# Optimization experiments

Hardware: AMD Instinct MI355X
Metric: run time of the kernel (lower is better)

Reference implementation:

```python
import jax, jax.numpy as jnp
import numpy as np

NUM_SEGMENTS = 50000  # number of graph nodes (max value in index)
NEG_SLOPE = 0.2


def setup_inputs() -> dict:
    key = jax.random.key(0)
    k1, k2, k3, k4, k5 = jax.random.split(key, 5)
    n_edges = 250000
    in_features = 128
    H, F = 8, 32
    messages = jax.random.normal(k1, (2 * n_edges, in_features), dtype=jnp.float32)
    W = jax.random.normal(k2, (H * F, in_features), dtype=jnp.float32) * (1.0 / np.sqrt(in_features))
    a_source = jax.random.normal(k3, (1, H, F), dtype=jnp.float32) * 0.1
    a_target = jax.random.normal(k4, (1, H, F), dtype=jnp.float32) * 0.1
    index = jax.random.randint(k5, (n_edges,), 0, NUM_SEGMENTS, dtype=jnp.int64)
    return {"messages": messages, "W": W, "a_source": a_source, "a_target": a_target, "index": index}


def _scatter_softmax(score, index):
    # score: [E, H]; index: [E] segment ids. Numerically stable softmax per segment.
    seg_max = jax.ops.segment_max(score, index, num_segments=NUM_SEGMENTS)  # [N, H]
    ex = jnp.exp(score - seg_max[index])
    denom = jax.ops.segment_sum(ex, index, num_segments=NUM_SEGMENTS)  # [N, H]
    return ex / (denom[index] + 1e-16)


def reference(messages, W, a_source, a_target, index):
    n_edges = index.shape[0]
    H, F = a_source.shape[1], a_source.shape[2]
    msg_src = messages[:n_edges]        # [E, in]
    msg_tgt = messages[n_edges:]        # [E, in]
    proj_src = (msg_src @ W.T).reshape(n_edges, H, F)  # [E, H, F]
    proj_tgt = (msg_tgt @ W.T).reshape(n_edges, H, F)
    score_src = jnp.sum(proj_src * a_source, axis=-1)  # [E, H]
    score_tgt = jnp.sum(proj_tgt * a_target, axis=-1)  # [E, H]
    score_edges = jax.nn.leaky_relu(score_src + score_tgt, negative_slope=NEG_SLOPE)
    att = _scatter_softmax(score_edges, index)         # [E, H]
    weighted = (att[..., None] * proj_tgt).reshape(n_edges, H * F)  # concat=True
    placeholder = proj_tgt.reshape(n_edges, H * F)
    return jnp.concatenate([weighted, placeholder], axis=0)  # [2E, H*F]
```

## Files before the change

### kernel.cpp

```cpp
#include <hip/hip_runtime.h>
#include <hip/hip_bf16.h>

#define NSEG 50000

typedef __attribute__((ext_vector_type(4))) float f32x4;
typedef __attribute__((ext_vector_type(8))) short s16x8;

static __device__ __forceinline__ unsigned short f2bf(float f) {
  unsigned int u = __float_as_uint(f);
  u += 0x7fffu + ((u >> 16) & 1u);
  return (unsigned short)(u >> 16);
}

static __device__ __forceinline__ s16x8 pack_bf16x8(const float* p) {
  float4 p0 = *(const float4*)(p);
  float4 p1 = *(const float4*)(p + 4);
  s16x8 v;
  v[0] = (short)f2bf(p0.x); v[1] = (short)f2bf(p0.y);
  v[2] = (short)f2bf(p0.z); v[3] = (short)f2bf(p0.w);
  v[4] = (short)f2bf(p1.x); v[5] = (short)f2bf(p1.y);
  v[6] = (short)f2bf(p1.z); v[7] = (short)f2bf(p1.w);
  return v;
}

__global__ __launch_bounds__(256) void prep_kernel(
    const float* __restrict__ W, const float* __restrict__ a_src,
    const float* __restrict__ a_tgt, unsigned short* __restrict__ Wb,
    unsigned short* __restrict__ wb_cat, float* __restrict__ denom) {
  int t = blockIdx.x * 256 + threadIdx.x;
  if (t < 32768) Wb[t] = f2bf(W[t]);
  if (t < 2048) {
    int row = t >> 7, k = t & 127;
    int h = row & 7;
    const float* a = (row < 8) ? a_src : a_tgt;
    float acc = 0.f;
    for (int f = 0; f < 32; ++f) acc += W[(h * 32 + f) * 128 + k] * a[h * 32 + f];
    wb_cat[t] = f2bf(acc);
  }
  if (t < NSEG * 8) denom[t] = 0.f;
}

__global__ __launch_bounds__(256) void score_kernel(
    const float* __restrict__ msg, const int* __restrict__ index,
    const unsigned short* __restrict__ wb_cat, float* __restrict__ ex,
    float* __restrict__ denom, int n) {
  int tid = threadIdx.x;
  int w = tid >> 6, l = tid & 63;
  int lcol = l & 15;
  int kgrp = l >> 4;
  int e0 = blockIdx.x * 64 + w * 16;
  int grow = e0 + lcol;
  int ga = grow < n ? grow : n - 1;
  const float* rs = msg + (size_t)ga * 128;
  const float* rt = msg + ((size_t)ga + (size_t)n) * 128;

  s16x8 afrag[4];
#pragma unroll
  for (int kk = 0; kk < 4; ++kk)
    afrag[kk] = *(const s16x8*)(wb_cat + lcol * 128 + kk * 32 + kgrp * 8);

  f32x4 ds = {0.f, 0.f, 0.f, 0.f};
  f32x4 dt = {0.f, 0.f, 0.f, 0.f};
#pragma unroll
  for (int kk = 0; kk < 4; ++kk) {
    int k0 = kk * 32 + kgrp * 8;
    s16x8 bs = pack_bf16x8(rs + k0);
    ds = __builtin_amdgcn_mfma_f32_16x16x32_bf16(afrag[kk], bs, ds, 0, 0, 0);
    s16x8 bt = pack_bf16x8(rt + k0);
    dt = __builtin_amdgcn_mfma_f32_16x16x32_bf16(afrag[kk], bt, dt, 0, 0, 0);
  }

  int ge = e0 + lcol;
  f32x4 evv;
#pragma unroll
  for (int r = 0; r < 4; ++r) {
    float tv = __shfl_xor(dt[r], 32);
    float s = ds[r] + tv;
    s = s > 0.f ? s : 0.2f * s;
    evv[r] = __expf(s);
  }
  if (kgrp < 2 && ge < n) {
    int seg = index[ge];
#pragma unroll
    for (int r = 0; r < 4; ++r) atomicAdd(&denom[seg * 8 + kgrp * 4 + r], evv[r]);
    *(f32x4*)(ex + (size_t)ge * 8 + kgrp * 4) = evv;
  }
}

__global__ __launch_bounds__(256) void gemm_kernel(
    const float* __restrict__ msg, const int* __restrict__ index,
    const unsigned short* __restrict__ Wb, const float* __restrict__ ex,
    const float* __restrict__ denom, float* __restrict__ out, int n) {
  __shared__ float att_lds[64][9];
  __shared__ float stg[2][16][260];
  int tid = threadIdx.x;
  int mbase = blockIdx.x * 64;

  for (int i = tid; i < 512; i += 256) {
    int r = i >> 3, h = i & 7;
    int ge = mbase + r;
    float a = 0.f;
    if (ge < n) {
      int seg = index[ge];
      a = ex[(size_t)ge * 8 + h] / (denom[seg * 8 + h] + 1e-16f);
    }
    att_lds[r][h] = a;
  }
  __syncthreads();

  int w = tid >> 6, l = tid & 63;
  int lcol = l & 15;
  int kgrp = l >> 4;

  s16x8 afrag[4][4];
#pragma unroll
  for (int ct = 0; ct < 4; ++ct) {
    int feat = w * 64 + ct * 16 + lcol;
#pragma unroll
    for (int kk = 0; kk < 4; ++kk)
      afrag[ct][kk] = *(const s16x8*)(Wb + (size_t)feat * 128 + kk * 32 + kgrp * 8);
  }

  for (int t = 0; t < 4; ++t) {
    int e0 = mbase + t * 16;
    int grow = e0 + lcol;
    int ga = grow < n ? grow : n - 1;
    const float* brow = msg + ((size_t)ga + (size_t)n) * 128;

    s16x8 bfrag[4];
#pragma unroll
    for (int kk = 0; kk < 4; ++kk) bfrag[kk] = pack_bf16x8(brow + kk * 32 + kgrp * 8);

#pragma unroll
    for (int ct = 0; ct < 4; ++ct) {
      f32x4 acc = {0.f, 0.f, 0.f, 0.f};
#pragma unroll
      for (int kk = 0; kk < 4; ++kk)
        acc = __builtin_amdgcn_mfma_f32_16x16x32_bf16(afrag[ct][kk], bfrag[kk], acc, 0, 0, 0);
      int f0 = w * 64 + ct * 16 + kgrp * 4;
      float a = att_lds[t * 16 + lcol][f0 >> 5];
      *(f32x4*)&stg[0][lcol][f0] = acc * a;
      *(f32x4*)&stg[1][lcol][f0] = acc;
    }
    asm volatile("s_waitcnt lgkmcnt(0)" ::: "memory");
    __builtin_amdgcn_s_barrier();

#pragma unroll
    for (int rnd = 0; rnd < 4; ++rnd) {
      int er = rnd * 4 + w;
      int ge = mbase + t * 16 + er;
      if (ge < n) {
        f32x4 v0 = *(const f32x4*)(&stg[0][er][0] + l * 4);
        __builtin_nontemporal_store(v0, (f32x4*)(out + (size_t)ge * 256 + l * 4));
        f32x4 v1 = *(const f32x4*)(&stg[1][er][0] + l * 4);
        __builtin_nontemporal_store(v1, (f32x4*)(out + ((size_t)ge + (size_t)n) * 256 + l * 4));
      }
    }
    asm volatile("s_waitcnt lgkmcnt(0)" ::: "memory");
    __builtin_amdgcn_s_barrier();
  }
}

extern "C" void kernel_launch(void* const* d_in, const int* in_sizes, int n_in,
                              void* d_out, int out_size, void* d_ws, size_t ws_size,
                              hipStream_t stream) {
  const float* messages = (const float*)d_in[0];
  const float* W        = (const float*)d_in[1];
  const float* a_src    = (const float*)d_in[2];
  const float* a_tgt    = (const float*)d_in[3];
  const int*   index    = (const int*)d_in[4];
  int n = in_sizes[4];

  char* ws = (char*)d_ws;
  unsigned short* Wb     = (unsigned short*)(ws);
  unsigned short* wb_cat = (unsigned short*)(ws + 65536);
  float* denom           = (float*)(ws + 69632);
  float* ex              = (float*)(ws + 69632 + 1600000);
  float* out = (float*)d_out;

  int nblk = (n + 63) / 64;
  prep_kernel<<<(NSEG * 8 + 255) / 256, 256, 0, stream>>>(W, a_src, a_tgt, Wb,
                                                          wb_cat, denom);
  score_kernel<<<nblk, 256, 0, stream>>>(messages, index, wb_cat, ex, denom, n);
  gemm_kernel<<<nblk, 256, 0, stream>>>(messages, index, Wb, ex, denom, out, n);
}
```

Measured before the change: 186.1 us.

## Fuse score and GEMM passes into one cooperative kernel with grid sync

After: 243.5 us. 1.31x slower.

```diff
diff --git a/kernel.cpp b/kernel.cpp
--- a/kernel.cpp
+++ b/kernel.cpp
@@ -1,7 +1,12 @@
 #include <hip/hip_runtime.h>
 #include <hip/hip_bf16.h>
+#include <hip/hip_cooperative_groups.h>
+
+namespace cg = cooperative_groups;
 
 #define NSEG 50000
+#define GRID 512
+#define CH 8
 
 typedef __attribute__((ext_vector_type(4))) float f32x4;
 typedef __attribute__((ext_vector_type(8))) short s16x8;
@@ -40,17 +45,149 @@
   if (t < NSEG * 8) denom[t] = 0.f;
 }
 
+__global__ __launch_bounds__(256, 2) void fused_kernel(
+    const float* __restrict__ msg, const int* __restrict__ index,
+    const unsigned short* __restrict__ Wb,
+    const unsigned short* __restrict__ wb_cat, float* __restrict__ denom,
+    float* __restrict__ out, int n) {
+  __shared__ unsigned short kv[4][4][64][8];
+  __shared__ float exl[CH][64][8];
+  __shared__ float att_lds[64][9];
+  __shared__ float stg[2][16][260];
+
+  int tid = threadIdx.x;
+  int w = tid >> 6, l = tid & 63;
+  int lcol = l & 15, kgrp = l >> 4;
+
+  s16x8 bfrag[CH][4];
+
+  {
+    s16x8 cfrag[4];
+#pragma unroll
+    for (int kk = 0; kk < 4; ++kk)
+      cfrag[kk] = *(const s16x8*)(wb_cat + lcol * 128 + kk * 32 + kgrp * 8);
+
+#pragma unroll
+    for (int c = 0; c < CH; ++c) {
+      int ge = (blockIdx.x * CH + c) * 64 + w * 16 + lcol;
+      int ga = ge < n ? ge : n - 1;
+      const float* rs = msg + (size_t)ga * 128;
+      const float* rt = msg + ((size_t)ga + (size_t)n) * 128;
+
+      f32x4 ds = {0.f, 0.f, 0.f, 0.f};
+      f32x4 dt = {0.f, 0.f, 0.f, 0.f};
+#pragma unroll
+      for (int kk = 0; kk < 4; ++kk) {
+        int k0 = kk * 32 + kgrp * 8;
+        s16x8 bs = pack_bf16x8(rs + k0);
+        ds = __builtin_amdgcn_mfma_f32_16x16x32_bf16(cfrag[kk], bs, ds, 0, 0, 0);
+        s16x8 bt = pack_bf16x8(rt + k0);
+        bfrag[c][kk] = bt;
+        dt = __builtin_amdgcn_mfma_f32_16x16x32_bf16(cfrag[kk], bt, dt, 0, 0, 0);
+      }
+
+      f32x4 evv;
+#pragma unroll
+      for (int r = 0; r < 4; ++r) {
+        float tv = __shfl_xor(dt[r], 32);
+        float s = ds[r] + tv;
+        s = s > 0.f ? s : 0.2f * s;
+        evv[r] = __expf(s);
+      }
+      if (kgrp < 2) {
+#pragma unroll
+        for (int r = 0; r < 4; ++r) exl[c][w * 16 + lcol][kgrp * 4 + r] = evv[r];
+        if (ge < n) {
+          int seg = index[ge];
+#pragma unroll
+          for (int r = 0; r < 4; ++r)
+            atomicAdd(&denom[seg * 8 + kgrp * 4 + r], evv[r]);
+        }
+      }
+    }
+  }
+
+  cg::this_grid().sync();
+
+  s16x8 afrag[4][4];
+#pragma unroll
+  for (int ct = 0; ct < 4; ++ct) {
+    int feat = w * 64 + ct * 16 + lcol;
+#pragma unroll
+    for (int kk = 0; kk < 4; ++kk)
+      afrag[ct][kk] = *(const s16x8*)(Wb + (size_t)feat * 128 + kk * 32 + kgrp * 8);
+  }
+
+#pragma unroll
+  for (int c = 0; c < CH; ++c) {
+    int ebase = (blockIdx.x * CH + c) * 64;
+
+#pragma unroll
+    for (int kk = 0; kk < 4; ++kk)
+      *(s16x8*)&kv[w][kk][l][0] = bfrag[c][kk];
+
+    for (int i = tid; i < 512; i += 256) {
+      int r = i >> 3, h = i & 7;
+      int ge2 = ebase + r;
+      float a = 0.f;
+      if (ge2 < n) {
+        int seg = index[ge2];
+        float dv = __hip_atomic_load(&denom[seg * 8 + h], __ATOMIC_RELAXED,
+                                     __HIP_MEMORY_SCOPE_AGENT);
+        a = exl[c][r][h] / (dv + 1e-16f);
+      }
+      att_lds[r][h] = a;
+    }
+    asm volatile("s_waitcnt lgkmcnt(0)" ::: "memory");
+    __builtin_amdgcn_s_barrier();
+
+#pragma unroll
+    for (int t = 0; t < 4; ++t) {
+      s16x8 bf[4];
+#pragma unroll
+      for (int kk = 0; kk < 4; ++kk) bf[kk] = *(const s16x8*)&kv[t][kk][l][0];
+
+#pragma unroll
+      for (int ct = 0; ct < 4; ++ct) {
+        f32x4 acc = {0.f, 0.f, 0.f, 0.f};
+#pragma unroll
+        for (int kk = 0; kk < 4; ++kk)
+          acc = __builtin_amdgcn_mfma_f32_16x16x32_bf16(afrag[ct][kk], bf[kk], acc, 0, 0, 0);
+        int f0 = w * 64 + ct * 16 + kgrp * 4;
+        float a = att_lds[t * 16 + lcol][f0 >> 5];
+        *(f32x4*)&stg[0][lcol][f0] = acc * a;
+        *(f32x4*)&stg[1][lcol][f0] = acc;
+      }
+      asm volatile("s_waitcnt lgkmcnt(0)" ::: "memory");
+      __builtin_amdgcn_s_barrier();
+
+#pragma unroll
+      for (int rnd = 0; rnd < 4; ++rnd) {
+        int er = rnd * 4 + w;
+        int ge2 = ebase + t * 16 + er;
+        if (ge2 < n) {
+          f32x4 v0 = *(const f32x4*)(&stg[0][er][0] + l * 4);
+          __builtin_nontemporal_store(v0, (f32x4*)(out + (size_t)ge2 * 256 + l * 4));
+          f32x4 v1 = *(const f32x4*)(&stg[1][er][0] + l * 4);
+          __builtin_nontemporal_store(
+              v1, (f32x4*)(out + ((size_t)ge2 + (size_t)n) * 256 + l * 4));
+        }
+      }
+      asm volatile("s_waitcnt lgkmcnt(0)" ::: "memory");
+      __builtin_amdgcn_s_barrier();
+    }
+  }
+}
+
 __global__ __launch_bounds__(256) void score_kernel(
     const float* __restrict__ msg, const int* __restrict__ index,
     const unsigned short* __restrict__ wb_cat, float* __restrict__ ex,
     float* __restrict__ denom, int n) {
   int tid = threadIdx.x;
   int w = tid >> 6, l = tid & 63;
-  int lcol = l & 15;
-  int kgrp = l >> 4;
-  int e0 = blockIdx.x * 64 + w * 16;
-  int grow = e0 + lcol;
-  int ga = grow < n ? grow : n - 1;
+  int lcol = l & 15, kgrp = l >> 4;
+  int ge = blockIdx.x * 64 + w * 16 + lcol;
+  int ga = ge < n ? ge : n - 1;
   const float* rs = msg + (size_t)ga * 128;
   const float* rt = msg + ((size_t)ga + (size_t)n) * 128;
 
@@ -70,7 +207,6 @@
     dt = __builtin_amdgcn_mfma_f32_16x16x32_bf16(afrag[kk], bt, dt, 0, 0, 0);
   }
 
-  int ge = e0 + lcol;
   f32x4 evv;
 #pragma unroll
   for (int r = 0; r < 4; ++r) {
@@ -109,8 +245,7 @@
   __syncthreads();
 
   int w = tid >> 6, l = tid & 63;
-  int lcol = l & 15;
-  int kgrp = l >> 4;
+  int lcol = l & 15, kgrp = l >> 4;
 
   s16x8 afrag[4][4];
 #pragma unroll
@@ -122,8 +257,7 @@
   }
 
   for (int t = 0; t < 4; ++t) {
-    int e0 = mbase + t * 16;
-    int grow = e0 + lcol;
+    int grow = mbase + t * 16 + lcol;
     int ga = grow < n ? grow : n - 1;
     const float* brow = msg + ((size_t)ga + (size_t)n) * 128;
 
@@ -178,9 +312,16 @@
   float* ex              = (float*)(ws + 69632 + 1600000);
   float* out = (float*)d_out;
 
-  int nblk = (n + 63) / 64;
   prep_kernel<<<(NSEG * 8 + 255) / 256, 256, 0, stream>>>(W, a_src, a_tgt, Wb,
                                                           wb_cat, denom);
-  score_kernel<<<nblk, 256, 0, stream>>>(messages, index, wb_cat, ex, denom, n);
-  gemm_kernel<<<nblk, 256, 0, stream>>>(messages, index, Wb, ex, denom, out, n);
-}
+
+  void* args[] = {(void*)&messages, (void*)&index, (void*)&Wb, (void*)&wb_cat,
+                  (void*)&denom, (void*)&out, (void*)&n};
+  hipError_t st = hipLaunchCooperativeKernel((void*)fused_kernel, dim3(GRID),
+                                             dim3(256), args, 0, stream);
+  if (st != hipSuccess) {
+    int nblk = (n + 63) / 64;
+    score_kernel<<<nblk, 256, 0, stream>>>(messages, index, wb_cat, ex, denom, n);
+    gemm_kernel<<<nblk, 256, 0, stream>>>(messages, index, Wb, ex, denom, out, n);
+  }
+}
```
